# Kernel optimization log

Measured on AMD Instinct MI355X. Metric: run time of the kernel, lower is better.

## Reference

```python
import jax, jax.numpy as jnp
import numpy as np

R = 1024          # number of 'a' tokens merged per sample
PROTECT_CLS = True


def setup_inputs() -> dict:
    key = jax.random.key(0)
    k1, k2 = jax.random.split(key)
    B, T, C = 8, 4096, 512
    x = jax.random.normal(k1, (B, T, C), dtype=jnp.float32)
    k = jax.random.normal(k2, (B, T, C), dtype=jnp.float32)
    return {"x": x, "k": k}


def reference(x, k):
    B, T, C = x.shape
    r = R
    pos_a = jnp.arange(0, T, 2)          # (Ta,)
    pos_b = jnp.arange(1, T, 2)          # (Tb,)
    Tb = pos_b.shape[0]

    # cosine-similarity scores between even ('a') and odd ('b') keys
    a = k[:, ::2, :]
    b = k[:, 1::2, :]
    a = a / (jnp.linalg.norm(a, axis=-1, keepdims=True) + 1e-12)
    b = b / (jnp.linalg.norm(b, axis=-1, keepdims=True) + 1e-12)
    scores = jnp.einsum('bac,bdc->bad', a, b)   # (B, Ta, Tb)
    if PROTECT_CLS:
        scores = scores.at[:, 0, :].set(-jnp.inf)

    node_max = jnp.max(scores, axis=-1)          # (B, Ta)
    node_idx = jnp.argmax(scores, axis=-1)       # (B, Ta) best 'b' partner per 'a'
    edge_order = jnp.argsort(-node_max, axis=-1) # descending
    src_idx = edge_order[:, :r]                  # merged 'a' tokens
    unm_sorted = jnp.sort(edge_order[:, r:], axis=-1)  # unmerged 'a', sorted
    dst_idx = jnp.take_along_axis(node_idx, src_idx, axis=-1)  # (B, r)

    src_tok = x[:, ::2, :]
    dst_tok = x[:, 1::2, :]
    unm = jnp.take_along_axis(src_tok, unm_sorted[..., None], axis=1)      # (B, Ta-r, C)
    src_sel = jnp.take_along_axis(src_tok, src_idx[..., None], axis=1)     # (B, r, C)
    dst_updated = jax.vmap(lambda d, i, s: d.at[i].add(s))(dst_tok, dst_idx, src_sel)
    merged = jnp.concatenate([unm, dst_updated], axis=1)                   # (B, Ta-r+Tb, C)

    base_b = unm.shape[1]
    unm_pos = pos_a[unm_sorted]   # (B, Ta-r) original positions of unmerged 'a'
    src_pos = pos_a[src_idx]      # (B, r)    original positions of merged 'a'

    def build_si(up, sp, di):
        si = jnp.full((T,), -1, dtype=jnp.int32)
        si = si.at[up].set(jnp.arange(base_b, dtype=jnp.int32))
        si = si.at[pos_b].set(base_b + jnp.arange(Tb, dtype=jnp.int32))
        si = si.at[sp].set((base_b + di).astype(jnp.int32))
        return si

    source_index = jax.vmap(build_si)(unm_pos, src_pos, dst_idx)  # (B, T)
    return merged, source_index
```

## Files before the change

kernel.cpp:

```cpp
#include <hip/hip_runtime.h>
#include <stdint.h>

#define BN 8
#define TN 4096
#define CN 512
#define TA 2048
#define RR 1024
#define BASEB 1024
#define MROWS 3072
#define KC 64
#define NCHUNK (CN / KC)
#define CAP 64

typedef _Float16 f16x8 __attribute__((ext_vector_type(8)));
typedef float f32x4 __attribute__((ext_vector_type(4)));
typedef __attribute__((address_space(3))) uint32_t lds_u32_t;
typedef __attribute__((address_space(1))) const uint32_t g_u32_t;

__device__ __forceinline__ unsigned ofloat(float f) {
    unsigned u = __float_as_uint(f);
    return (u & 0x80000000u) ? ~u : (u | 0x80000000u);
}
__device__ __forceinline__ float unofloat(unsigned u) {
    unsigned v = (u & 0x80000000u) ? (u ^ 0x80000000u) : ~u;
    return __uint_as_float(v);
}

__global__ __launch_bounds__(256) void split_kernel(const float* __restrict__ k,
        _Float16* __restrict__ Ahi, _Float16* __restrict__ Bhi,
        float* __restrict__ invA, float* __restrict__ invB,
        float* __restrict__ nHa, float* __restrict__ nLa,
        float* __restrict__ Pq, float* __restrict__ Qq,
        unsigned long long* __restrict__ nodekey,
        int* __restrict__ cnt, unsigned* __restrict__ maxHH) {
    int row = blockIdx.x * 4 + (threadIdx.x >> 6);
    int lane = threadIdx.x & 63;
    const float* p = k + (size_t)row * CN;
    float4 v1 = *(const float4*)(p + lane * 8);
    float4 v2 = *(const float4*)(p + lane * 8 + 4);
    float s = v1.x*v1.x + v1.y*v1.y + v1.z*v1.z + v1.w*v1.w
            + v2.x*v2.x + v2.y*v2.y + v2.z*v2.z + v2.w*v2.w;
    #pragma unroll
    for (int off = 32; off > 0; off >>= 1) s += __shfl_xor(s, off);
    float inv = 1.0f / (sqrtf(s) + 1e-12f);
    float sc = 1024.0f * inv;
    float m[8] = {v1.x*sc, v1.y*sc, v1.z*sc, v1.w*sc,
                  v2.x*sc, v2.y*sc, v2.z*sc, v2.w*sc};
    f16x8 H;
    float h2 = 0.f, l2 = 0.f;
    #pragma unroll
    for (int jj = 0; jj < 8; ++jj) {
        _Float16 h = (_Float16)m[jj];
        H[jj] = h;
        float hf = (float)h;
        float lf = m[jj] - hf;
        h2 += hf * hf;
        l2 += lf * lf;
    }
    #pragma unroll
    for (int off = 32; off > 0; off >>= 1) {
        h2 += __shfl_xor(h2, off);
        l2 += __shfl_xor(l2, off);
    }
    float nh = sqrtf(h2), nl = sqrtf(l2);
    int b = row >> 12;
    int tt = row & 4095;
    int node = tt >> 1;
    size_t dst = (((size_t)(b * NCHUNK + (lane >> 3)) * TA + node)) * KC
               + (lane & 7) * 8;
    if (tt & 1) {
        *(f16x8*)(Bhi + dst) = H;
        if (lane == 0) {
            invB[b * TA + node] = inv;
            Pq[b * TA + node] = nl + 1.2f + 4e-5f * nh;
            Qq[b * TA + node] = nh + nl + 1050.0f;
            nodekey[b * TA + node] =
                (((unsigned long long)0x007FFFFFu) << 32) | 0xFFFFFFFFull;
            cnt[b * TA + node] = 0;
            maxHH[b * TA + node] = 0u;
        }
    } else {
        *(f16x8*)(Ahi + dst) = H;
        if (lane == 0) {
            invA[b * TA + node] = inv;
            nHa[b * TA + node] = nh;
            nLa[b * TA + node] = nl;
        }
    }
}

__global__ __launch_bounds__(256, 4) void score_hh_kernel(
        const _Float16* __restrict__ Ahi, const _Float16* __restrict__ Bhi,
        const float* __restrict__ nHa, const float* __restrict__ nLa,
        const float* __restrict__ Pq, const float* __restrict__ Qq,
        int* __restrict__ cnt, unsigned* __restrict__ maxHH,
        int* __restrict__ candJ, float* __restrict__ candS) {
    __shared__ _Float16 lds[2 * 128 * KC];
    __shared__ float rowmax2[128][2];
    const int lid = blockIdx.x;
    const int b  = lid & 7;
    const int t  = lid >> 3;
    const int i0 = (t & 15) << 7;
    const int j0 = (t >> 4) << 7;
    const int tid = threadIdx.x;
    const int lane = tid & 63;
    const int w = tid >> 6;
    const int wr = (w >> 1) * 64;
    const int wc = (w & 1) * 64;

    const size_t chunkstride = (size_t)TA * KC;
    const size_t batchbase = (size_t)b * NCHUNK * chunkstride;
    const _Float16* pbase[2] = { Ahi + batchbase + (size_t)i0 * KC,
                                 Bhi + batchbase + (size_t)j0 * KC };
    int srcoff[8];
    #pragma unroll
    for (int i = 0; i < 8; ++i) {
        int s = (i & 3) * 256 + tid;
        int n = s >> 3, sg = s & 7;
        srcoff[i] = n * KC + ((sg ^ (n & 7)) * 8);
    }

    f32x4 acc[4][4];
    #pragma unroll
    for (int m = 0; m < 4; ++m)
        #pragma unroll
        for (int n = 0; n < 4; ++n) acc[m][n] = (f32x4){0.f, 0.f, 0.f, 0.f};

    const int fr = lane & 15, ks = lane >> 4;
    int rowbaseA[4], rowbaseB[4];
    #pragma unroll
    for (int m = 0; m < 4; ++m) rowbaseA[m] = (wr + m * 16 + fr) * KC;
    #pragma unroll
    for (int n = 0; n < 4; ++n) rowbaseB[n] = (wc + n * 16 + fr) * KC;

    for (int kt = 0; kt < NCHUNK; ++kt) {
        const size_t cb = (size_t)kt * chunkstride;
        #pragma unroll
        for (int i = 0; i < 8; ++i) {
            _Float16* lp = lds + (i >> 2) * 8192 + ((i & 3) * 256 + tid) * 8;
            __builtin_amdgcn_global_load_lds(
                (g_u32_t*)(pbase[i >> 2] + cb + srcoff[i]),
                (lds_u32_t*)lp, 16, 0, 0);
        }
        __syncthreads();
        #pragma unroll
        for (int kk = 0; kk < 2; ++kk) {
            const int slo = (((kk << 2) + ks) ^ (fr & 7)) * 8;
            f16x8 bh[4];
            #pragma unroll
            for (int n = 0; n < 4; ++n)
                bh[n] = *(const f16x8*)(&lds[8192 + rowbaseB[n] + slo]);
            #pragma unroll
            for (int m = 0; m < 4; ++m) {
                f16x8 ah = *(const f16x8*)(&lds[rowbaseA[m] + slo]);
                #pragma unroll
                for (int n = 0; n < 4; ++n)
                    acc[m][n] = __builtin_amdgcn_mfma_f32_16x16x32_f16(ah, bh[n], acc[m][n], 0, 0, 0);
            }
        }
        __syncthreads();
    }

    float wmax[4][4];
    #pragma unroll
    for (int m = 0; m < 4; ++m)
        #pragma unroll
        for (int reg = 0; reg < 4; ++reg) {
            float mx = acc[m][0][reg];
            #pragma unroll
            for (int n = 1; n < 4; ++n) mx = fmaxf(mx, acc[m][n][reg]);
            #pragma unroll
            for (int mm2 = 8; mm2 > 0; mm2 >>= 1)
                mx = fmaxf(mx, __shfl_xor(mx, mm2, 16));
            wmax[m][reg] = mx;
        }
    if (fr == 0) {
        #pragma unroll
        for (int m = 0; m < 4; ++m)
            #pragma unroll
            for (int reg = 0; reg < 4; ++reg) {
                int r = wr + m * 16 + ks * 4 + reg;
                rowmax2[r][w & 1] = wmax[m][reg];
            }
    }
    __syncthreads();
    if (fr == 0) {
        #pragma unroll
        for (int m = 0; m < 4; ++m)
            #pragma unroll
            for (int reg = 0; reg < 4; ++reg) {
                int r = wr + m * 16 + ks * 4 + reg;
                atomicMax(&maxHH[b * TA + i0 + r], ofloat(wmax[m][reg]));
            }
    }
    float Pj[4], Qj[4];
    #pragma unroll
    for (int n = 0; n < 4; ++n) {
        int j = j0 + wc + n * 16 + fr;
        Pj[n] = Pq[b * TA + j];
        Qj[n] = Qq[b * TA + j];
    }
    #pragma unroll
    for (int m = 0; m < 4; ++m)
        #pragma unroll
        for (int reg = 0; reg < 4; ++reg) {
            int r = wr + m * 16 + ks * 4 + reg;
            int i = i0 + r;
            float M = fmaxf(rowmax2[r][0], rowmax2[r][1]);
            float ha = nHa[b * TA + i], la = nLa[b * TA + i];
            #pragma unroll
            for (int n = 0; n < 4; ++n) {
                float s = acc[m][n][reg];
                if (s >= M - (ha * Pj[n] + la * Qj[n])) {
                    int j = j0 + wc + n * 16 + fr;
                    int idx = atomicAdd(&cnt[b * TA + i], 1);
                    if (idx < CAP) {
                        candJ[(size_t)(b * TA + i) * CAP + idx] = j;
                        candS[(size_t)(b * TA + i) * CAP + idx] = s;
                    }
                }
            }
        }
}

__global__ __launch_bounds__(256) void rescore_kernel(const float* __restrict__ k,
        const float* __restrict__ invA, const float* __restrict__ invB,
        const float* __restrict__ nHa, const float* __restrict__ nLa,
        const float* __restrict__ Pq, const float* __restrict__ Qq,
        const int* __restrict__ cnt, const unsigned* __restrict__ maxHH,
        const int* __restrict__ candJ, const float* __restrict__ candS,
        unsigned long long* __restrict__ nodekey) {
    const int b = blockIdx.y;
    const int wv = threadIdx.x >> 6;
    const int lane = threadIdx.x & 63;
    const int i = blockIdx.x * 4 + wv;
    if (i == 0) return;
    const size_t base = (size_t)b * TA;
    float inva = invA[base + i];
    const float* ka = k + ((size_t)b * TN + 2 * i) * CN + lane * 8;
    float a[8];
    #pragma unroll
    for (int e = 0; e < 8; ++e) a[e] = ka[e] * inva;
    int c_n = cnt[base + i];
    float gmax = unofloat(maxHH[base + i]);
    float ha = nHa[base + i], la = nLa[base + i];
    unsigned bhi = 0u, blo = 0u;

    if (c_n <= CAP) {
        for (int c = 0; c < c_n; ++c) {
            int j = candJ[(base + i) * CAP + c];
            float s = candS[(base + i) * CAP + c];
            if (s < gmax - (ha * Pq[base + j] + la * Qq[base + j])) continue;
            float invb = invB[base + j];
            const float* kb = k + ((size_t)b * TN + 2 * j + 1) * CN + lane * 8;
            float d = 0.f;
            #pragma unroll
            for (int e = 0; e < 8; ++e) d += a[e] * (kb[e] * invb);
            #pragma unroll
            for (int off = 32; off > 0; off >>= 1) d += __shfl_xor(d, off);
            unsigned khi = ofloat(d), klo = 0xFFFFFFFFu - (unsigned)j;
            if (khi > bhi || (khi == bhi && klo > blo)) { bhi = khi; blo = klo; }
        }
    } else {
        for (int j = 0; j < TA; ++j) {
            float invb = invB[base + j];
            const float* kb = k + ((size_t)b * TN + 2 * j + 1) * CN + lane * 8;
            float d = 0.f;
            #pragma unroll
            for (int e = 0; e < 8; ++e) d += a[e] * (kb[e] * invb);
            #pragma unroll
            for (int off = 32; off > 0; off >>= 1) d += __shfl_xor(d, off);
            unsigned khi = ofloat(d), klo = 0xFFFFFFFFu - (unsigned)j;
            if (khi > bhi || (khi == bhi && klo > blo)) { bhi = khi; blo = klo; }
        }
    }
    if (lane == 0)
        nodekey[base + i] = (((unsigned long long)bhi) << 32) | blo;
}

__global__ __launch_bounds__(256) void rank_flag_kernel(
        const unsigned long long* __restrict__ nodekey,
        int* __restrict__ is_src) {
    __shared__ unsigned long long K[2048];
    const int b = blockIdx.y;
    const int t = threadIdx.x;
    for (int i = t; i < 2048; i += 256) {
        unsigned hi = (unsigned)(nodekey[b * TA + i] >> 32);
        K[i] = (((unsigned long long)hi) << 32) | (unsigned)(2047 - i);
    }
    __syncthreads();
    const int i = blockIdx.x * 256 + t;
    const unsigned long long ki = K[i];
    int rank = 0;
    #pragma unroll 8
    for (int j = 0; j < 2048; ++j) rank += (K[j] > ki) ? 1 : 0;
    is_src[b * TA + i] = (rank < RR) ? 1 : 0;
}

__global__ __launch_bounds__(1024) void scan_si_kernel(const int* __restrict__ is_src,
        const unsigned long long* __restrict__ nodekey,
        int* __restrict__ unm_rank, float* __restrict__ out_si) {
    __shared__ int ps[2048];
    __shared__ unsigned char fl[2048];
    const int b = blockIdx.x;
    const int t = threadIdx.x;
    int s0 = is_src[b * TA + t];
    int s1 = is_src[b * TA + 1024 + t];
    int f0 = 1 - s0, f1 = 1 - s1;
    fl[t] = (unsigned char)s0;
    fl[t + 1024] = (unsigned char)s1;
    ps[t] = f0;
    ps[t + 1024] = f1;
    __syncthreads();
    for (int off = 1; off < 2048; off <<= 1) {
        int v0 = (t >= off) ? ps[t - off] : 0;
        int v1 = ((t + 1024) >= off) ? ps[t + 1024 - off] : 0;
        __syncthreads();
        ps[t] += v0;
        ps[t + 1024] += v1;
        __syncthreads();
    }
    int u0 = ps[t] - f0, u1 = ps[t + 1024] - f1;
    unm_rank[b * TA + t] = u0;
    unm_rank[b * TA + 1024 + t] = u1;
    #pragma unroll
    for (int h = 0; h < 2; ++h) {
        int i = t + h * 1024;
        int u = h ? u1 : u0;
        int val;
        if (fl[i]) {
            unsigned j = 0xFFFFFFFFu - (unsigned)(nodekey[b * TA + i] & 0xFFFFFFFFull);
            val = BASEB + (int)j;
        } else {
            val = u;
        }
        out_si[(size_t)b * TN + 2 * i]     = (float)val;
        out_si[(size_t)b * TN + 2 * i + 1] = (float)(BASEB + i);
    }
}

__global__ __launch_bounds__(128) void copy_kernel(const float* __restrict__ x,
                                                   const int* __restrict__ is_src,
                                                   const int* __restrict__ unm_rank,
                                                   float* __restrict__ out) {
    const int b = blockIdx.y;
    const int tt = blockIdx.x;
    const float* src;
    float* dst;
    if (tt < 2048) {
        int i = tt;
        if (is_src[b * TA + i]) return;
        src = x + ((size_t)b * TN + 2 * i) * CN;
        dst = out + ((size_t)b * MROWS + unm_rank[b * TA + i]) * CN;
    } else {
        int j = tt - 2048;
        src = x + ((size_t)b * TN + 2 * j + 1) * CN;
        dst = out + ((size_t)b * MROWS + BASEB + j) * CN;
    }
    ((float4*)dst)[threadIdx.x] = ((const float4*)src)[threadIdx.x];
}

__global__ __launch_bounds__(256) void scatter_kernel(const float* __restrict__ x,
                                                      const int* __restrict__ is_src,
                                                      const unsigned long long* __restrict__ nodekey,
                                                      float* __restrict__ out) {
    const int b = blockIdx.y;
    const int i = blockIdx.x;
    if (!is_src[b * TA + i]) return;
    unsigned j = 0xFFFFFFFFu - (unsigned)(nodekey[b * TA + i] & 0xFFFFFFFFull);
    const float* src = x + ((size_t)b * TN + 2 * i) * CN;
    float* dst = out + ((size_t)b * MROWS + BASEB + j) * CN;
    for (int c = threadIdx.x; c < CN; c += 256) atomicAdd(&dst[c], src[c]);
}

extern "C" void kernel_launch(void* const* d_in, const int* in_sizes, int n_in,
                              void* d_out, int out_size, void* d_ws, size_t ws_size,
                              hipStream_t stream) {
    const float* x = (const float*)d_in[0];
    const float* k = (const float*)d_in[1];
    float* out = (float*)d_out;
    float* out_si = out + (size_t)BN * MROWS * CN;

    char* ws = (char*)d_ws;
    const size_t PLANE = (size_t)BN * TA * CN;
    _Float16* Ahi = (_Float16*)ws;
    _Float16* Bhi = Ahi + PLANE;
    char* tail = ws + 2 * PLANE * sizeof(_Float16);
    const size_t NN = (size_t)BN * TA;
    float* invA = (float*)(tail);
    float* invB = invA + NN;
    float* nHa  = invB + NN;
    float* nLa  = nHa + NN;
    float* Pq   = nLa + NN;
    float* Qq   = Pq + NN;
    unsigned long long* nodekey = (unsigned long long*)(Qq + NN);
    int* cnt        = (int*)(nodekey + NN);
    unsigned* maxHH = (unsigned*)(cnt + NN);
    int* is_src     = (int*)(maxHH + NN);
    int* unm_rank   = is_src + NN;
    int* candJ      = unm_rank + NN;
    float* candS    = (float*)(candJ + NN * CAP);

    split_kernel<<<dim3(BN * TN / 4), dim3(256), 0, stream>>>(
        k, Ahi, Bhi, invA, invB, nHa, nLa, Pq, Qq, nodekey, cnt, maxHH);
    score_hh_kernel<<<dim3(2048), dim3(256), 0, stream>>>(
        Ahi, Bhi, nHa, nLa, Pq, Qq, cnt, maxHH, candJ, candS);
    rescore_kernel<<<dim3(512, BN), dim3(256), 0, stream>>>(
        k, invA, invB, nHa, nLa, Pq, Qq, cnt, maxHH, candJ, candS, nodekey);
    rank_flag_kernel<<<dim3(8, BN), dim3(256), 0, stream>>>(nodekey, is_src);
    scan_si_kernel<<<dim3(BN), dim3(1024), 0, stream>>>(is_src, nodekey, unm_rank, out_si);
    copy_kernel<<<dim3(4096, BN), dim3(128), 0, stream>>>(x, is_src, unm_rank, out);
    scatter_kernel<<<dim3(2048, BN), dim3(256), 0, stream>>>(x, is_src, nodekey, out);
}
```

Before: 196.1 us.

## Replace copy plus atomic scatter with gather-based merge using per-destination source lists

The scan kernel now builds a rank-to-node map for unmerged tokens and a per-destination list of merged source indices, capped at a fixed size. A single move kernel then writes each output row once: unmerged rows by gather, and destination rows by summing the base token with its listed sources in registers. This removes the float atomicAdd scatter pass and the early-exiting blocks of the old copy kernel. Lists that overflow the cap fall back to a serial per-thread atomic kernel, which would be slow when one destination receives many sources. Summation order also changes.

```diff
diff --git a/kernel.cpp b/kernel.cpp
--- a/kernel.cpp
+++ b/kernel.cpp
@@ -11,6 +11,7 @@
 #define KC 64
 #define NCHUNK (CN / KC)
 #define CAP 64
+#define DCAP 32
 
 typedef _Float16 f16x8 __attribute__((ext_vector_type(8)));
 typedef float f32x4 __attribute__((ext_vector_type(4)));
@@ -32,7 +33,8 @@
         float* __restrict__ nHa, float* __restrict__ nLa,
         float* __restrict__ Pq, float* __restrict__ Qq,
         unsigned long long* __restrict__ nodekey,
-        int* __restrict__ cnt, unsigned* __restrict__ maxHH) {
+        int* __restrict__ cnt, unsigned* __restrict__ maxHH,
+        int* __restrict__ dcnt) {
     int row = blockIdx.x * 4 + (threadIdx.x >> 6);
     int lane = threadIdx.x & 63;
     const float* p = k + (size_t)row * CN;
@@ -78,6 +80,7 @@
                 (((unsigned long long)0x007FFFFFu) << 32) | 0xFFFFFFFFull;
             cnt[b * TA + node] = 0;
             maxHH[b * TA + node] = 0u;
+            dcnt[b * TA + node] = 0;
         }
     } else {
         *(f16x8*)(Ahi + dst) = H;
@@ -299,7 +302,9 @@
 
 __global__ __launch_bounds__(1024) void scan_si_kernel(const int* __restrict__ is_src,
         const unsigned long long* __restrict__ nodekey,
-        int* __restrict__ unm_rank, float* __restrict__ out_si) {
+        float* __restrict__ out_si, int* __restrict__ rank2node,
+        int* __restrict__ dcnt, int* __restrict__ dlist,
+        int* __restrict__ aidx) {
     __shared__ int ps[2048];
     __shared__ unsigned char fl[2048];
     const int b = blockIdx.x;
@@ -321,8 +326,6 @@
         __syncthreads();
     }
     int u0 = ps[t] - f0, u1 = ps[t + 1024] - f1;
-    unm_rank[b * TA + t] = u0;
-    unm_rank[b * TA + 1024 + t] = u1;
     #pragma unroll
     for (int h = 0; h < 2; ++h) {
         int i = t + h * 1024;
@@ -331,46 +334,56 @@
         if (fl[i]) {
             unsigned j = 0xFFFFFFFFu - (unsigned)(nodekey[b * TA + i] & 0xFFFFFFFFull);
             val = BASEB + (int)j;
+            int idx = atomicAdd(&dcnt[b * TA + (int)j], 1);
+            aidx[b * TA + i] = idx;
+            if (idx < DCAP)
+                dlist[((size_t)b * TA + (int)j) * DCAP + idx] = i;
         } else {
             val = u;
+            rank2node[b * BASEB + u] = i;
         }
         out_si[(size_t)b * TN + 2 * i]     = (float)val;
         out_si[(size_t)b * TN + 2 * i + 1] = (float)(BASEB + i);
     }
 }
 
-__global__ __launch_bounds__(128) void copy_kernel(const float* __restrict__ x,
-                                                   const int* __restrict__ is_src,
-                                                   const int* __restrict__ unm_rank,
-                                                   float* __restrict__ out) {
+__global__ __launch_bounds__(128) void move_kernel(const float* __restrict__ x,
+        const int* __restrict__ rank2node, const int* __restrict__ dcnt,
+        const int* __restrict__ dlist, float* __restrict__ out) {
     const int b = blockIdx.y;
-    const int tt = blockIdx.x;
-    const float* src;
-    float* dst;
-    if (tt < 2048) {
-        int i = tt;
-        if (is_src[b * TA + i]) return;
-        src = x + ((size_t)b * TN + 2 * i) * CN;
-        dst = out + ((size_t)b * MROWS + unm_rank[b * TA + i]) * CN;
+    const int r = blockIdx.x;
+    float4* dst = (float4*)(out + ((size_t)b * MROWS + r) * CN);
+    if (r < BASEB) {
+        int i = rank2node[b * BASEB + r];
+        const float4* src = (const float4*)(x + ((size_t)b * TN + 2 * i) * CN);
+        dst[threadIdx.x] = src[threadIdx.x];
     } else {
-        int j = tt - 2048;
-        src = x + ((size_t)b * TN + 2 * j + 1) * CN;
-        dst = out + ((size_t)b * MROWS + BASEB + j) * CN;
-    }
-    ((float4*)dst)[threadIdx.x] = ((const float4*)src)[threadIdx.x];
-}
-
-__global__ __launch_bounds__(256) void scatter_kernel(const float* __restrict__ x,
-                                                      const int* __restrict__ is_src,
-                                                      const unsigned long long* __restrict__ nodekey,
-                                                      float* __restrict__ out) {
+        int j = r - BASEB;
+        const float4* sd = (const float4*)(x + ((size_t)b * TN + 2 * j + 1) * CN);
+        float4 v = sd[threadIdx.x];
+        int c = dcnt[b * TA + j];
+        if (c > DCAP) c = DCAP;
+        for (int s = 0; s < c; ++s) {
+            int i = dlist[((size_t)b * TA + j) * DCAP + s];
+            const float4* ss = (const float4*)(x + ((size_t)b * TN + 2 * i) * CN);
+            float4 w = ss[threadIdx.x];
+            v.x += w.x; v.y += w.y; v.z += w.z; v.w += w.w;
+        }
+        dst[threadIdx.x] = v;
+    }
+}
+
+__global__ __launch_bounds__(256) void overflow_kernel(const float* __restrict__ x,
+        const int* __restrict__ is_src, const int* __restrict__ aidx,
+        const unsigned long long* __restrict__ nodekey,
+        float* __restrict__ out) {
     const int b = blockIdx.y;
-    const int i = blockIdx.x;
-    if (!is_src[b * TA + i]) return;
+    const int i = blockIdx.x * 256 + threadIdx.x;
+    if (!is_src[b * TA + i] || aidx[b * TA + i] < DCAP) return;
     unsigned j = 0xFFFFFFFFu - (unsigned)(nodekey[b * TA + i] & 0xFFFFFFFFull);
     const float* src = x + ((size_t)b * TN + 2 * i) * CN;
     float* dst = out + ((size_t)b * MROWS + BASEB + j) * CN;
-    for (int c = threadIdx.x; c < CN; c += 256) atomicAdd(&dst[c], src[c]);
+    for (int c = 0; c < CN; ++c) atomicAdd(&dst[c], src[c]);
 }
 
 extern "C" void kernel_launch(void* const* d_in, const int* in_sizes, int n_in,
@@ -397,18 +410,24 @@
     int* cnt        = (int*)(nodekey + NN);
     unsigned* maxHH = (unsigned*)(cnt + NN);
     int* is_src     = (int*)(maxHH + NN);
-    int* unm_rank   = is_src + NN;
-    int* candJ      = unm_rank + NN;
+    int* dcnt       = is_src + NN;
+    int* aidx       = dcnt + NN;
+    int* rank2node  = aidx + NN;
+    int* candJ      = rank2node + (size_t)BN * BASEB;
     float* candS    = (float*)(candJ + NN * CAP);
+    int* dlist      = (int*)(candS + NN * CAP);
 
     split_kernel<<<dim3(BN * TN / 4), dim3(256), 0, stream>>>(
-        k, Ahi, Bhi, invA, invB, nHa, nLa, Pq, Qq, nodekey, cnt, maxHH);
+        k, Ahi, Bhi, invA, invB, nHa, nLa, Pq, Qq, nodekey, cnt, maxHH, dcnt);
     score_hh_kernel<<<dim3(2048), dim3(256), 0, stream>>>(
         Ahi, Bhi, nHa, nLa, Pq, Qq, cnt, maxHH, candJ, candS);
     rescore_kernel<<<dim3(512, BN), dim3(256), 0, stream>>>(
         k, invA, invB, nHa, nLa, Pq, Qq, cnt, maxHH, candJ, candS, nodekey);
     rank_flag_kernel<<<dim3(8, BN), dim3(256), 0, stream>>>(nodekey, is_src);
-    scan_si_kernel<<<dim3(BN), dim3(1024), 0, stream>>>(is_src, nodekey, unm_rank, out_si);
-    copy_kernel<<<dim3(4096, BN), dim3(128), 0, stream>>>(x, is_src, unm_rank, out);
-    scatter_kernel<<<dim3(2048, BN), dim3(256), 0, stream>>>(x, is_src, nodekey, out);
-}
+    scan_si_kernel<<<dim3(BN), dim3(1024), 0, stream>>>(
+        is_src, nodekey, out_si, rank2node, dcnt, dlist, aidx);
+    move_kernel<<<dim3(MROWS, BN), dim3(128), 0, stream>>>(
+        x, rank2node, dcnt, dlist, out);
+    overflow_kernel<<<dim3(TA / 256, BN), dim3(256), 0, stream>>>(
+        x, is_src, aidx, nodekey, out);
+}
```

Measured after the change: 182.2 us, median of 2. -7.0%, faster.
